# Performance work log

Hardware: AMD Instinct MI355X
Metric: run time of the kernel (lower is better)

Reference implementation:

```python
import jax, jax.numpy as jnp
import numpy as np

N_STATE, N_OBS, BATCH, T_LEN = 256, 128, 64, 1024
RICCATI_ITERS = 300


def _steady_state_gain(A, H, Q, R, iters=RICCATI_ITERS):
    """Riccati iteration for the steady-state Kalman gain (numpy, fp64)."""
    n = A.shape[0]
    I = np.eye(n)
    P = np.eye(n)
    for _ in range(iters):
        Pp = A @ P @ A.T + Q
        S = H @ Pp @ H.T + R
        K = np.linalg.solve(S, (Pp @ H.T).T).T
        P = (I - K @ H) @ Pp
    return K


def setup_inputs() -> dict:
    rng = np.random.default_rng(0)
    # Stable dynamics: scaled orthogonal matrix (spectral radius 0.95).
    M = rng.standard_normal((N_STATE, N_STATE))
    Qm, _ = np.linalg.qr(M)
    A = 0.95 * Qm
    H = rng.standard_normal((N_OBS, N_STATE)) / np.sqrt(N_STATE)
    Qc = 0.1 * np.eye(N_STATE)
    Rc = 0.1 * np.eye(N_OBS)
    K = _steady_state_gain(A, H, Qc, Rc)

    key = jax.random.key(0)
    y = jax.random.normal(key, (BATCH, T_LEN, N_OBS), dtype=jnp.float32)
    return {
        "y": y,
        "A": jnp.asarray(A, dtype=jnp.float32),
        "H": jnp.asarray(H, dtype=jnp.float32),
        "K": jnp.asarray(K, dtype=jnp.float32),
    }


def reference(y, A, H, K):
    """Steady-state Kalman filter: x_t = (I - K H) A x_{t-1} + K y_t.

    y: [B, T, n_obs] -> out: [B, T, n_state]
    """
    n = A.shape[0]
    I = jnp.eye(n, dtype=A.dtype)
    A_eff = (I - K @ H) @ A  # [n, n]

    x0 = y[:, 0] @ K.T  # [B, n]

    def step(x, yt):
        x = x @ A_eff.T + yt @ K.T  # [B, n]
        return x, x

    ys = jnp.swapaxes(y[:, 1:], 0, 1)  # [T-1, B, n_obs]
    _, xs = jax.lax.scan(step, x0, ys)  # xs: [T-1, B, n]
    out = jnp.concatenate([x0[:, None, :], jnp.swapaxes(xs, 0, 1)], axis=1)
    return out  # [B, T, n_state]
```

## Files before the change

### kernel.cpp

```cpp
#include <hip/hip_runtime.h>
#include <hip/hip_bf16.h>

#define NS 256
#define MO 128
#define BB 64
#define TT 1024
#define CCH 64
#define SS 16

typedef short s16x8 __attribute__((ext_vector_type(8)));
typedef float f32x4 __attribute__((ext_vector_type(4)));
typedef unsigned int uint;
typedef unsigned short ushort;

__device__ __forceinline__ ushort f2bf(float x) {
    uint u = __float_as_uint(x);
    uint r = (u + 0x7fffu + ((u >> 16) & 1u)) >> 16;
    return (ushort)r;
}
__device__ __forceinline__ float bf2f(ushort h) { return __uint_as_float(((uint)h) << 16); }

__device__ __forceinline__ uint pkbf2(float a, float b) {
    __hip_bfloat162 h = __float22bfloat162_rn(make_float2(a, b));
    union { __hip_bfloat162 b2; uint u; } cv;
    cv.b2 = h;
    return cv.u;
}

__device__ __forceinline__ void conv8(float4 f0, float4 f1, s16x8& vh, s16x8& vl) {
    uint h0 = pkbf2(f0.x, f0.y), h1 = pkbf2(f0.z, f0.w);
    uint h2 = pkbf2(f1.x, f1.y), h3 = pkbf2(f1.z, f1.w);
    float r0 = f0.x - __uint_as_float(h0 << 16);
    float r1 = f0.y - __uint_as_float(h0 & 0xffff0000u);
    float r2 = f0.z - __uint_as_float(h1 << 16);
    float r3 = f0.w - __uint_as_float(h1 & 0xffff0000u);
    float r4 = f1.x - __uint_as_float(h2 << 16);
    float r5 = f1.y - __uint_as_float(h2 & 0xffff0000u);
    float r6 = f1.z - __uint_as_float(h3 << 16);
    float r7 = f1.w - __uint_as_float(h3 & 0xffff0000u);
    uint l0 = pkbf2(r0, r1), l1 = pkbf2(r2, r3);
    uint l2 = pkbf2(r4, r5), l3 = pkbf2(r6, r7);
    union { uint u[4]; s16x8 v; } ch, cl;
    ch.u[0] = h0; ch.u[1] = h1; ch.u[2] = h2; ch.u[3] = h3;
    cl.u[0] = l0; cl.u[1] = l1; cl.u[2] = l2; cl.u[3] = l3;
    vh = ch.v; vl = cl.v;
}

__device__ __forceinline__ f32x4 mfma16(s16x8 a, s16x8 b, f32x4 c) {
    return __builtin_amdgcn_mfma_f32_16x16x32_bf16(a, b, c, 0, 0, 0);
}


__global__ void kh_kernel(const float* __restrict__ K, const float* __restrict__ H,
                          float* __restrict__ KH) {
    int i = blockIdx.x, j = threadIdx.x;
    __shared__ float kl[MO];
    if (j < MO) kl[j] = K[i * MO + j];
    __syncthreads();
    float acc = 0.f;
#pragma unroll 8
    for (int k = 0; k < MO; ++k) acc += kl[k] * H[k * NS + j];
    KH[i * NS + j] = acc;
}

__global__ void aeff_kernel(const float* __restrict__ A, const float* __restrict__ KH,
                            float* __restrict__ AE) {
    int i = blockIdx.x, j = threadIdx.x;
    __shared__ float khr[NS];
    khr[j] = KH[i * NS + j];
    __syncthreads();
    float acc = A[i * NS + j];
#pragma unroll 8
    for (int k = 0; k < NS; ++k) acc -= khr[k] * A[k * NS + j];
    AE[i * NS + j] = acc;
}

__global__ void matsq_kernel(const float* __restrict__ src, float* __restrict__ dst) {
    int i = blockIdx.x, j = threadIdx.x;
    __shared__ float row[NS];
    row[j] = src[i * NS + j];
    __syncthreads();
    float acc = 0.f;
#pragma unroll 8
    for (int k = 0; k < NS; ++k) acc += row[k] * src[k * NS + j];
    dst[i * NS + j] = acc;
}

__global__ void conv_kernel(const float* __restrict__ AE, const float* __restrict__ M,
                            const float* __restrict__ M2, const float* __restrict__ K,
                            ushort* __restrict__ aeh, ushort* __restrict__ ael,
                            ushort* __restrict__ mh, ushort* __restrict__ ml,
                            ushort* __restrict__ m2h, ushort* __restrict__ m2l,
                            ushort* __restrict__ kbh, ushort* __restrict__ kbl) {
    int blk = blockIdx.x;
    if (blk >= 768) {
        int i = (blk - 768) * 256 + threadIdx.x;
        float v = K[i];
        ushort hi = f2bf(v);
        kbh[i] = hi;
        kbl[i] = f2bf(v - bf2f(hi));
        return;
    }
    int i = (blk & 255) * 256 + threadIdx.x;
    int mat = blk >> 8;
    const float* src = (mat == 0) ? AE : ((mat == 1) ? M : M2);
    ushort* dh = (mat == 0) ? aeh : ((mat == 1) ? mh : m2h);
    ushort* dl = (mat == 0) ? ael : ((mat == 1) ? ml : m2l);
    float v = src[i];
    ushort hi = f2bf(v);
    dh[i] = hi;
    dl[i] = f2bf(v - bf2f(hi));
}


template <int MODE>
__launch_bounds__(512, 2)
__global__ void scan16_kernel(const ushort* __restrict__ mh, const ushort* __restrict__ ml,
                              const ushort* __restrict__ kbh, const ushort* __restrict__ kbl,
                              const float* __restrict__ y_g,
                              const float* u, const float* __restrict__ cin,
                              float* wout, float* __restrict__ eout) {
    constexpr bool YF = (MODE == 0 || MODE == 4);
    constexpr int S = YF ? SS : 8;
    const int tid = threadIdx.x;
    const int blk = blockIdx.x;
    const int w = tid >> 6;
    const int l = tid & 63;
    const int lr = l & 15;
    const int lg = l >> 4;

    __shared__ ushort xh_s[16 * NS];
    __shared__ ushort xl_s[16 * NS];
    __shared__ float ybuf[2][16 * MO];
    __shared__ float xe_s[16 * NS];

    const int b0 = (blk & 3) * 16;
    const int cc = blk >> 2;
    const int t0 = cc * SS;

    auto ubase = [&](int m) -> long {
        if constexpr (MODE == 1 || MODE == 3) {
            int rid = blk * 16 + m;
            int b = rid >> 3, g = rid & 7;
            return ((long)b * 64 + g * 8) * NS;
        } else {
            int b = blk * 16 + m;
            return (long)b * 8 * NS;
        }
    };

    s16x8 Bh[2][8], Bl[2][8];
#pragma unroll
    for (int t2 = 0; t2 < 2; ++t2) {
        int row = 16 * (2 * w + t2) + lr;
#pragma unroll
        for (int q = 0; q < 8; ++q) {
            int off = row * NS + 32 * q + 8 * lg;
            Bh[t2][q] = *(const s16x8*)(mh + off);
            Bl[t2][q] = *(const s16x8*)(ml + off);
        }
    }

    s16x8 KBh[2][4], KBl[2][4];
    if constexpr (YF) {
#pragma unroll
        for (int t2 = 0; t2 < 2; ++t2) {
            int row = 16 * (2 * w + t2) + lr;
#pragma unroll
            for (int q = 0; q < 4; ++q) {
                int off = row * MO + 32 * q + 8 * lg;
                KBh[t2][q] = *(const s16x8*)(kbh + off);
                KBl[t2][q] = *(const s16x8*)(kbl + off);
            }
        }
    }

#pragma unroll
    for (int jj = 0; jj < 8; ++jj) {
        int idx = jj * 512 + tid;
        int m = idx >> 8, col = idx & 255;
        float xv = 0.f;
        if constexpr (MODE == 3) {
            int rid = blk * 16 + m;
            int b = rid >> 3, g = rid & 7;
            xv = cin[(b * 8 + g) * NS + col];
            if (g == 0) wout[(long)b * 64 * NS + col] = 0.f;
        } else if constexpr (MODE == 4) {
            xv = cin[((long)(b0 + m) * 64 + cc) * NS + col];
        } else if constexpr (MODE == 2) {
            int b = blk * 16 + m;
            wout[(long)b * 8 * NS + col] = 0.f;
        }
        ushort hi = f2bf(xv);
        ushort lo = f2bf(xv - bf2f(hi));
        int sidx = (m * NS + col) ^ ((m & 7) << 3);
        xh_s[sidx] = hi;
        xl_s[sidx] = lo;
    }

    const int col0 = 32 * w + lr;
    const int col1 = col0 + 16;

    const int yr = tid >> 5;
    const int yc = (tid & 31) << 2;
    const float* ysrc = nullptr;
    int ywbyte = 0;
    float4 vnext = make_float4(0.f, 0.f, 0.f, 0.f);
    if constexpr (YF) {
        ysrc = y_g + ((size_t)(b0 + yr) * TT + t0) * MO + yc;
        ywbyte = (yr * 512 + yc * 4) ^ ((yr & 7) << 4);
        float4 v0 = *(const float4*)(ysrc);
        *(float4*)((char*)(&ybuf[0][0]) + ywbyte) = v0;
        vnext = *(const float4*)(ysrc + MO);
    }

    float up0[4], up1[4];
    if constexpr (!YF) {
#pragma unroll
        for (int i = 0; i < 4; ++i) {
            int m = 4 * lg + i;
            long ub = ubase(m);
            up0[i] = u[ub + col0];
            up1[i] = u[ub + col1];
        }
    }
    __syncthreads();

    for (int s = 0; s < S; ++s) {
        f32x4 acc0, acc1;
        if constexpr (YF) {
            acc0 = f32x4{0.f, 0.f, 0.f, 0.f};
            acc1 = f32x4{0.f, 0.f, 0.f, 0.f};
            const char* yb = (const char*)(&ybuf[s & 1][0]);
#pragma unroll
            for (int q = 0; q < 4; ++q) {
                int lb = lr * 512 + q * 128 + lg * 32;
                float4 f0 = *(const float4*)(yb + (lb ^ ((lr & 7) << 4)));
                float4 f1 = *(const float4*)(yb + ((lb + 16) ^ ((lr & 7) << 4)));
                s16x8 yh, yl;
                conv8(f0, f1, yh, yl);
                acc0 = mfma16(yh, KBh[0][q], acc0);
                acc0 = mfma16(yl, KBh[0][q], acc0);
                acc0 = mfma16(yh, KBl[0][q], acc0);
                acc1 = mfma16(yh, KBh[1][q], acc1);
                acc1 = mfma16(yl, KBh[1][q], acc1);
                acc1 = mfma16(yh, KBl[1][q], acc1);
            }
        } else {
            acc0[0] = up0[0]; acc0[1] = up0[1]; acc0[2] = up0[2]; acc0[3] = up0[3];
            acc1[0] = up1[0]; acc1[1] = up1[1]; acc1[2] = up1[2]; acc1[3] = up1[3];
        }

#pragma unroll
        for (int q = 0; q < 8; ++q) {
            int ridx = (lr * NS + 32 * q + 8 * lg) ^ ((lr & 7) << 3);
            s16x8 xh = *(const s16x8*)&xh_s[ridx];
            s16x8 xl = *(const s16x8*)&xl_s[ridx];
            acc0 = mfma16(xh, Bh[0][q], acc0);
            acc0 = mfma16(xl, Bh[0][q], acc0);
            acc0 = mfma16(xh, Bl[0][q], acc0);
            acc1 = mfma16(xh, Bh[1][q], acc1);
            acc1 = mfma16(xl, Bh[1][q], acc1);
            acc1 = mfma16(xh, Bl[1][q], acc1);
        }

        if constexpr (!YF) {
            if (s + 1 < S) {
#pragma unroll
                for (int i = 0; i < 4; ++i) {
                    int m = 4 * lg + i;
                    long ub = ubase(m) + (long)(s + 1) * NS;
                    up0[i] = u[ub + col0];
                    up1[i] = u[ub + col1];
                }
            }
        }

        if constexpr (MODE == 2) {
            if (s < 7) {
#pragma unroll
                for (int i = 0; i < 4; ++i) {
                    int m = 4 * lg + i;
                    int b = blk * 16 + m;
                    long wb = ((long)b * 8 + s + 1) * NS;
                    wout[wb + col0] = acc0[i];
                    wout[wb + col1] = acc1[i];
                }
            }
        } else if constexpr (MODE == 3) {
#pragma unroll
            for (int i = 0; i < 4; ++i) {
                int m = 4 * lg + i;
                int rid = blk * 16 + m;
                int b = rid >> 3, g = rid & 7;
                int kk = 8 * g + s + 1;
                if (kk < 64) {
                    long wb = ((long)b * 64 + kk) * NS;
                    wout[wb + col0] = acc0[i];
                    wout[wb + col1] = acc1[i];
                }
            }
        }
        if constexpr (MODE == 0 || MODE == 1) {
            if (s == S - 1) {
#pragma unroll
                for (int i = 0; i < 4; ++i) {
                    int m = 4 * lg + i;
                    long eb;
                    if constexpr (MODE == 0) {
                        eb = ((long)(b0 + m) * 64 + cc) * NS;
                    } else {
                        eb = (long)(blk * 16 + m) * NS;
                    }
                    eout[eb + col0] = acc0[i];
                    eout[eb + col1] = acc1[i];
                }
            }
        }

        __syncthreads();

#pragma unroll
        for (int i = 0; i < 4; ++i) {
            int m = 4 * lg + i;
            {
                ushort hi = f2bf(acc0[i]);
                ushort lo = f2bf(acc0[i] - bf2f(hi));
                int wi = (m * NS + col0) ^ ((m & 7) << 3);
                xh_s[wi] = hi;
                xl_s[wi] = lo;
            }
            {
                ushort hi = f2bf(acc1[i]);
                ushort lo = f2bf(acc1[i] - bf2f(hi));
                int wi = (m * NS + col1) ^ ((m & 7) << 3);
                xh_s[wi] = hi;
                xl_s[wi] = lo;
            }
            if constexpr (MODE == 4) {
                xe_s[(m * NS + col0) ^ ((m & 7) << 2)] = acc0[i];
                xe_s[(m * NS + col1) ^ ((m & 7) << 2)] = acc1[i];
            }
        }
        if constexpr (YF) {
            if (s + 1 < S) {
                *(float4*)((char*)(&ybuf[(s + 1) & 1][0]) + ywbyte) = vnext;
                if (s + 2 < S) vnext = *(const float4*)(ysrc + (size_t)(s + 2) * MO);
            }
        }
        __syncthreads();

        if constexpr (MODE == 4) {
#pragma unroll
            for (int j = 0; j < 2; ++j) {
                int idx = j * 512 + tid;
                int r = idx >> 6;
                int wb = idx << 2;
                float4 vv = *(const float4*)&xe_s[wb ^ ((r & 7) << 2)];
                long ob = ((long)(b0 + r) * TT + (t0 + s)) * NS + (wb & 255);
                *(float4*)(wout + ob) = vv;
            }
        }
    }
}


extern "C" void kernel_launch(void* const* d_in, const int* in_sizes, int n_in,
                              void* d_out, int out_size, void* d_ws, size_t ws_size,
                              hipStream_t stream) {
    const float* y = (const float*)d_in[0];
    const float* A = (const float*)d_in[1];
    const float* H = (const float*)d_in[2];
    const float* K = (const float*)d_in[3];
    float* out = (float*)d_out;

    float* ws = (float*)d_ws;
    const long MAT = (long)NS * NS;
    float* KH = ws + 0 * MAT;
    float* AE = ws + 1 * MAT;
    float* W0 = ws + 2 * MAT;
    float* W1 = ws + 3 * MAT;
    float* W2 = ws + 4 * MAT;
    float* W3 = ws + 5 * MAT;
    float* W4 = ws + 6 * MAT;
    float* W5 = ws + 7 * MAT;
    float* W6 = ws + 8 * MAT;
    ushort* aeh = (ushort*)(ws + 9 * MAT);
    ushort* ael = aeh + MAT;
    ushort* mh = ael + MAT;
    ushort* ml = mh + MAT;
    ushort* m2h = ml + MAT;
    ushort* m2l = m2h + MAT;
    ushort* kbh = (ushort*)(ws + 12 * MAT);
    ushort* kbl = kbh + (long)NS * MO;
    float* e_buf = ws + 13 * MAT;
    float* e2 = ws + 29 * MAT;
    float* c2 = ws + 31 * MAT;
    float* cbuf = ws + 33 * MAT;

    kh_kernel<<<NS, NS, 0, stream>>>(K, H, KH);
    aeff_kernel<<<NS, NS, 0, stream>>>(A, KH, AE);
    matsq_kernel<<<NS, NS, 0, stream>>>(AE, W0);
    matsq_kernel<<<NS, NS, 0, stream>>>(W0, W1);
    matsq_kernel<<<NS, NS, 0, stream>>>(W1, W2);
    matsq_kernel<<<NS, NS, 0, stream>>>(W2, W3);
    matsq_kernel<<<NS, NS, 0, stream>>>(W3, W4);
    matsq_kernel<<<NS, NS, 0, stream>>>(W4, W5);
    matsq_kernel<<<NS, NS, 0, stream>>>(W5, W6);
    conv_kernel<<<896, 256, 0, stream>>>(AE, W3, W6, K, aeh, ael, mh, ml, m2h, m2l, kbh, kbl);

    scan16_kernel<0><<<256, 512, 0, stream>>>(aeh, ael, kbh, kbl, y, nullptr, nullptr, nullptr, e_buf);
    scan16_kernel<1><<<32, 512, 0, stream>>>(mh, ml, nullptr, nullptr, nullptr, e_buf, nullptr, nullptr, e2);
    scan16_kernel<2><<<4, 512, 0, stream>>>(m2h, m2l, nullptr, nullptr, nullptr, e2, nullptr, c2, nullptr);
    scan16_kernel<3><<<32, 512, 0, stream>>>(mh, ml, nullptr, nullptr, nullptr, e_buf, c2, cbuf, nullptr);
    scan16_kernel<4><<<256, 512, 0, stream>>>(aeh, ael, kbh, kbl, y, nullptr, cbuf, out, nullptr);
}
```

Measured before the change: 272.4 us.

## Restructure hierarchical scan: precompute input GEMM, chunk of 8, bf16 carries, double-buffered LDS

```diff
diff --git a/kernel.cpp b/kernel.cpp
--- a/kernel.cpp
+++ b/kernel.cpp
@@ -5,8 +5,6 @@
 #define MO 128
 #define BB 64
 #define TT 1024
-#define CCH 64
-#define SS 16
 
 typedef short s16x8 __attribute__((ext_vector_type(8)));
 typedef float f32x4 __attribute__((ext_vector_type(4)));
@@ -52,10 +50,17 @@
 
 
 __global__ void kh_kernel(const float* __restrict__ K, const float* __restrict__ H,
-                          float* __restrict__ KH) {
+                          float* __restrict__ KH,
+                          ushort* __restrict__ kbh, ushort* __restrict__ kbl) {
     int i = blockIdx.x, j = threadIdx.x;
     __shared__ float kl[MO];
-    if (j < MO) kl[j] = K[i * MO + j];
+    if (j < MO) {
+        float v = K[i * MO + j];
+        kl[j] = v;
+        ushort hi = f2bf(v);
+        kbh[i * MO + j] = hi;
+        kbl[i * MO + j] = f2bf(v - bf2f(hi));
+    }
     __syncthreads();
     float acc = 0.f;
 #pragma unroll 8
@@ -64,7 +69,8 @@
 }
 
 __global__ void aeff_kernel(const float* __restrict__ A, const float* __restrict__ KH,
-                            float* __restrict__ AE) {
+                            float* __restrict__ AE,
+                            ushort* __restrict__ aeh, ushort* __restrict__ ael) {
     int i = blockIdx.x, j = threadIdx.x;
     __shared__ float khr[NS];
     khr[j] = KH[i * NS + j];
@@ -73,9 +79,13 @@
 #pragma unroll 8
     for (int k = 0; k < NS; ++k) acc -= khr[k] * A[k * NS + j];
     AE[i * NS + j] = acc;
-}
-
-__global__ void matsq_kernel(const float* __restrict__ src, float* __restrict__ dst) {
+    ushort hi = f2bf(acc);
+    aeh[i * NS + j] = hi;
+    ael[i * NS + j] = f2bf(acc - bf2f(hi));
+}
+
+__global__ void matsq_kernel(const float* __restrict__ src, float* __restrict__ dst,
+                             ushort* dh, ushort* dl) {
     int i = blockIdx.x, j = threadIdx.x;
     __shared__ float row[NS];
     row[j] = src[i * NS + j];
@@ -84,70 +94,91 @@
 #pragma unroll 8
     for (int k = 0; k < NS; ++k) acc += row[k] * src[k * NS + j];
     dst[i * NS + j] = acc;
-}
-
-__global__ void conv_kernel(const float* __restrict__ AE, const float* __restrict__ M,
-                            const float* __restrict__ M2, const float* __restrict__ K,
-                            ushort* __restrict__ aeh, ushort* __restrict__ ael,
-                            ushort* __restrict__ mh, ushort* __restrict__ ml,
-                            ushort* __restrict__ m2h, ushort* __restrict__ m2l,
-                            ushort* __restrict__ kbh, ushort* __restrict__ kbl) {
-    int blk = blockIdx.x;
-    if (blk >= 768) {
-        int i = (blk - 768) * 256 + threadIdx.x;
-        float v = K[i];
-        ushort hi = f2bf(v);
-        kbh[i] = hi;
-        kbl[i] = f2bf(v - bf2f(hi));
-        return;
-    }
-    int i = (blk & 255) * 256 + threadIdx.x;
-    int mat = blk >> 8;
-    const float* src = (mat == 0) ? AE : ((mat == 1) ? M : M2);
-    ushort* dh = (mat == 0) ? aeh : ((mat == 1) ? mh : m2h);
-    ushort* dl = (mat == 0) ? ael : ((mat == 1) ? ml : m2l);
-    float v = src[i];
-    ushort hi = f2bf(v);
-    dh[i] = hi;
-    dl[i] = f2bf(v - bf2f(hi));
+    if (dh) {
+        ushort hi = f2bf(acc);
+        dh[i * NS + j] = hi;
+        dl[i * NS + j] = f2bf(acc - bf2f(hi));
+    }
+}
+
+
+__launch_bounds__(512, 4)
+__global__ void ugemm_kernel(const float* __restrict__ y, const ushort* __restrict__ kbh,
+                             const ushort* __restrict__ kbl, float* __restrict__ U) {
+    const int tid = threadIdx.x, blk = blockIdx.x;
+    const int w = tid >> 6, l = tid & 63, lr = l & 15, lg = l >> 4;
+
+    __shared__ float xe[16 * NS];
+
+    s16x8 KBh[2][4], KBl[2][4];
+#pragma unroll
+    for (int t2 = 0; t2 < 2; ++t2) {
+        int row = 16 * (2 * w + t2) + lr;
+#pragma unroll
+        for (int q = 0; q < 4; ++q) {
+            int off = row * MO + 32 * q + 8 * lg;
+            KBh[t2][q] = *(const s16x8*)(kbh + off);
+            KBl[t2][q] = *(const s16x8*)(kbl + off);
+        }
+    }
+
+#pragma unroll 1
+    for (int it = 0; it < 8; ++it) {
+        long row0 = ((long)blk * 8 + it) * 16;
+        s16x8 Ah[4], Al[4];
+#pragma unroll
+        for (int q = 0; q < 4; ++q) {
+            long off = (row0 + lr) * MO + 32 * q + 8 * lg;
+            float4 f0 = *(const float4*)(y + off);
+            float4 f1 = *(const float4*)(y + off + 4);
+            conv8(f0, f1, Ah[q], Al[q]);
+        }
+        f32x4 acc0 = {0.f, 0.f, 0.f, 0.f};
+        f32x4 acc1 = {0.f, 0.f, 0.f, 0.f};
+#pragma unroll
+        for (int q = 0; q < 4; ++q) {
+            acc0 = mfma16(Ah[q], KBh[0][q], acc0);
+            acc0 = mfma16(Al[q], KBh[0][q], acc0);
+            acc0 = mfma16(Ah[q], KBl[0][q], acc0);
+            acc1 = mfma16(Ah[q], KBh[1][q], acc1);
+            acc1 = mfma16(Al[q], KBh[1][q], acc1);
+            acc1 = mfma16(Ah[q], KBl[1][q], acc1);
+        }
+        const int col0 = 32 * w + lr, col1 = col0 + 16;
+#pragma unroll
+        for (int i = 0; i < 4; ++i) {
+            int m = 4 * lg + i;
+            xe[(m * NS + col0) ^ ((m & 7) << 2)] = acc0[i];
+            xe[(m * NS + col1) ^ ((m & 7) << 2)] = acc1[i];
+        }
+        __syncthreads();
+#pragma unroll
+        for (int j = 0; j < 2; ++j) {
+            int idx = j * 512 + tid;
+            int r = idx >> 6;
+            int wb = idx << 2;
+            float4 v = *(const float4*)&xe[wb ^ ((r & 7) << 2)];
+            *(float4*)(U + (row0 + r) * NS + (wb & 255)) = v;
+        }
+        __syncthreads();
+    }
 }
 
 
 template <int MODE>
-__launch_bounds__(512, 2)
+__launch_bounds__(512, 4)
 __global__ void scan16_kernel(const ushort* __restrict__ mh, const ushort* __restrict__ ml,
-                              const ushort* __restrict__ kbh, const ushort* __restrict__ kbl,
-                              const float* __restrict__ y_g,
-                              const float* u, const float* __restrict__ cin,
-                              float* wout, float* __restrict__ eout) {
-    constexpr bool YF = (MODE == 0 || MODE == 4);
-    constexpr int S = YF ? SS : 8;
-    const int tid = threadIdx.x;
-    const int blk = blockIdx.x;
-    const int w = tid >> 6;
-    const int l = tid & 63;
-    const int lr = l & 15;
-    const int lg = l >> 4;
-
-    __shared__ ushort xh_s[16 * NS];
-    __shared__ ushort xl_s[16 * NS];
-    __shared__ float ybuf[2][16 * MO];
-    __shared__ float xe_s[16 * NS];
-
-    const int b0 = (blk & 3) * 16;
-    const int cc = blk >> 2;
-    const int t0 = cc * SS;
-
-    auto ubase = [&](int m) -> long {
-        if constexpr (MODE == 1 || MODE == 3) {
-            int rid = blk * 16 + m;
-            int b = rid >> 3, g = rid & 7;
-            return ((long)b * 64 + g * 8) * NS;
-        } else {
-            int b = blk * 16 + m;
-            return (long)b * 8 * NS;
-        }
-    };
+                              const float* __restrict__ uf, const ushort* __restrict__ ub,
+                              const ushort* __restrict__ cin, float* __restrict__ outf,
+                              ushort* __restrict__ wbf, ushort* __restrict__ ebf) {
+    constexpr int S = (MODE == 2) ? 15 : ((MODE == 3) ? 7 : 8);
+    constexpr bool UF32 = (MODE == 0 || MODE == 4);
+    const int tid = threadIdx.x, blk = blockIdx.x;
+    const int w = tid >> 6, l = tid & 63, lr = l & 15, lg = l >> 4;
+
+    __shared__ ushort xh_s[2][16 * NS];
+    __shared__ ushort xl_s[2][16 * NS];
+    __shared__ float xe_s[(MODE == 4) ? 2 * 16 * NS : 4];
 
     s16x8 Bh[2][8], Bl[2][8];
 #pragma unroll
@@ -161,101 +192,70 @@
         }
     }
 
-    s16x8 KBh[2][4], KBl[2][4];
-    if constexpr (YF) {
-#pragma unroll
-        for (int t2 = 0; t2 < 2; ++t2) {
-            int row = 16 * (2 * w + t2) + lr;
-#pragma unroll
-            for (int q = 0; q < 4; ++q) {
-                int off = row * MO + 32 * q + 8 * lg;
-                KBh[t2][q] = *(const s16x8*)(kbh + off);
-                KBl[t2][q] = *(const s16x8*)(kbl + off);
-            }
-        }
-    }
-
 #pragma unroll
     for (int jj = 0; jj < 8; ++jj) {
         int idx = jj * 512 + tid;
         int m = idx >> 8, col = idx & 255;
-        float xv = 0.f;
+        ushort hu = 0;
         if constexpr (MODE == 3) {
             int rid = blk * 16 + m;
-            int b = rid >> 3, g = rid & 7;
-            xv = cin[(b * 8 + g) * NS + col];
-            if (g == 0) wout[(long)b * 64 * NS + col] = 0.f;
+            int b = rid >> 4, g = rid & 15;
+            hu = cin[((long)b * 16 + g) * NS + col];
+            wbf[((long)b * 128 + g * 8) * NS + col] = hu;
         } else if constexpr (MODE == 4) {
-            xv = cin[((long)(b0 + m) * 64 + cc) * NS + col];
+            int b = (blk & 3) * 16 + m, cc = blk >> 2;
+            hu = cin[((long)b * 128 + cc) * NS + col];
         } else if constexpr (MODE == 2) {
             int b = blk * 16 + m;
-            wout[(long)b * 8 * NS + col] = 0.f;
-        }
-        ushort hi = f2bf(xv);
-        ushort lo = f2bf(xv - bf2f(hi));
-        int sidx = (m * NS + col) ^ ((m & 7) << 3);
-        xh_s[sidx] = hi;
-        xl_s[sidx] = lo;
-    }
-
-    const int col0 = 32 * w + lr;
-    const int col1 = col0 + 16;
-
-    const int yr = tid >> 5;
-    const int yc = (tid & 31) << 2;
-    const float* ysrc = nullptr;
-    int ywbyte = 0;
-    float4 vnext = make_float4(0.f, 0.f, 0.f, 0.f);
-    if constexpr (YF) {
-        ysrc = y_g + ((size_t)(b0 + yr) * TT + t0) * MO + yc;
-        ywbyte = (yr * 512 + yc * 4) ^ ((yr & 7) << 4);
-        float4 v0 = *(const float4*)(ysrc);
-        *(float4*)((char*)(&ybuf[0][0]) + ywbyte) = v0;
-        vnext = *(const float4*)(ysrc + MO);
+            wbf[(long)b * 16 * NS + col] = 0;
+        }
+        int si = (m * NS + col) ^ ((m & 7) << 3);
+        xh_s[0][si] = hu;
+        xl_s[0][si] = 0;
+    }
+
+    const int col0 = 32 * w + lr, col1 = col0 + 16;
+    const int m0 = 4 * lg;
+
+    long ubo[4];
+#pragma unroll
+    for (int i = 0; i < 4; ++i) {
+        int m = m0 + i;
+        if constexpr (UF32) {
+            int b = (blk & 3) * 16 + m, cc = blk >> 2;
+            ubo[i] = ((long)b * TT + cc * 8) * NS;
+        } else if constexpr (MODE == 1 || MODE == 3) {
+            int rid = blk * 16 + m;
+            ubo[i] = ((long)(rid >> 4) * 128 + (rid & 15) * 8) * NS;
+        } else {
+            ubo[i] = (long)(blk * 16 + m) * 16 * NS;
+        }
     }
 
     float up0[4], up1[4];
-    if constexpr (!YF) {
-#pragma unroll
-        for (int i = 0; i < 4; ++i) {
-            int m = 4 * lg + i;
-            long ub = ubase(m);
-            up0[i] = u[ub + col0];
-            up1[i] = u[ub + col1];
+#pragma unroll
+    for (int i = 0; i < 4; ++i) {
+        if constexpr (UF32) {
+            up0[i] = uf[ubo[i] + col0];
+            up1[i] = uf[ubo[i] + col1];
+        } else {
+            up0[i] = bf2f(ub[ubo[i] + col0]);
+            up1[i] = bf2f(ub[ubo[i] + col1]);
         }
     }
     __syncthreads();
 
     for (int s = 0; s < S; ++s) {
+        const int cur = s & 1, nxt = cur ^ 1;
         f32x4 acc0, acc1;
-        if constexpr (YF) {
-            acc0 = f32x4{0.f, 0.f, 0.f, 0.f};
-            acc1 = f32x4{0.f, 0.f, 0.f, 0.f};
-            const char* yb = (const char*)(&ybuf[s & 1][0]);
-#pragma unroll
-            for (int q = 0; q < 4; ++q) {
-                int lb = lr * 512 + q * 128 + lg * 32;
-                float4 f0 = *(const float4*)(yb + (lb ^ ((lr & 7) << 4)));
-                float4 f1 = *(const float4*)(yb + ((lb + 16) ^ ((lr & 7) << 4)));
-                s16x8 yh, yl;
-                conv8(f0, f1, yh, yl);
-                acc0 = mfma16(yh, KBh[0][q], acc0);
-                acc0 = mfma16(yl, KBh[0][q], acc0);
-                acc0 = mfma16(yh, KBl[0][q], acc0);
-                acc1 = mfma16(yh, KBh[1][q], acc1);
-                acc1 = mfma16(yl, KBh[1][q], acc1);
-                acc1 = mfma16(yh, KBl[1][q], acc1);
-            }
-        } else {
-            acc0[0] = up0[0]; acc0[1] = up0[1]; acc0[2] = up0[2]; acc0[3] = up0[3];
-            acc1[0] = up1[0]; acc1[1] = up1[1]; acc1[2] = up1[2]; acc1[3] = up1[3];
-        }
+        acc0[0] = up0[0]; acc0[1] = up0[1]; acc0[2] = up0[2]; acc0[3] = up0[3];
+        acc1[0] = up1[0]; acc1[1] = up1[1]; acc1[2] = up1[2]; acc1[3] = up1[3];
 
 #pragma unroll
         for (int q = 0; q < 8; ++q) {
             int ridx = (lr * NS + 32 * q + 8 * lg) ^ ((lr & 7) << 3);
-            s16x8 xh = *(const s16x8*)&xh_s[ridx];
-            s16x8 xl = *(const s16x8*)&xl_s[ridx];
+            s16x8 xh = *(const s16x8*)&xh_s[cur][ridx];
+            s16x8 xl = *(const s16x8*)&xl_s[cur][ridx];
             acc0 = mfma16(xh, Bh[0][q], acc0);
             acc0 = mfma16(xl, Bh[0][q], acc0);
             acc0 = mfma16(xh, Bl[0][q], acc0);
@@ -264,101 +264,93 @@
             acc1 = mfma16(xh, Bl[1][q], acc1);
         }
 
-        if constexpr (!YF) {
-            if (s + 1 < S) {
+        if (s + 1 < S) {
+#pragma unroll
+            for (int i = 0; i < 4; ++i) {
+                long ue = ubo[i] + (long)(s + 1) * NS;
+                if constexpr (UF32) {
+                    up0[i] = uf[ue + col0];
+                    up1[i] = uf[ue + col1];
+                } else {
+                    up0[i] = bf2f(ub[ue + col0]);
+                    up1[i] = bf2f(ub[ue + col1]);
+                }
+            }
+        }
+
+        if constexpr (MODE == 2) {
+#pragma unroll
+            for (int i = 0; i < 4; ++i) {
+                int b = blk * 16 + m0 + i;
+                long wb = ((long)b * 16 + s + 1) * NS;
+                wbf[wb + col0] = f2bf(acc0[i]);
+                wbf[wb + col1] = f2bf(acc1[i]);
+            }
+        } else if constexpr (MODE == 3) {
+#pragma unroll
+            for (int i = 0; i < 4; ++i) {
+                int rid = blk * 16 + m0 + i;
+                int b = rid >> 4, g = rid & 15;
+                long wb = ((long)b * 128 + g * 8 + s + 1) * NS;
+                wbf[wb + col0] = f2bf(acc0[i]);
+                wbf[wb + col1] = f2bf(acc1[i]);
+            }
+        } else if constexpr (MODE == 0) {
+            if (s == S - 1) {
 #pragma unroll
                 for (int i = 0; i < 4; ++i) {
-                    int m = 4 * lg + i;
-                    long ub = ubase(m) + (long)(s + 1) * NS;
-                    up0[i] = u[ub + col0];
-                    up1[i] = u[ub + col1];
+                    int b = (blk & 3) * 16 + m0 + i, cc = blk >> 2;
+                    long eb = ((long)b * 128 + cc) * NS;
+                    ebf[eb + col0] = f2bf(acc0[i]);
+                    ebf[eb + col1] = f2bf(acc1[i]);
                 }
             }
-        }
-
-        if constexpr (MODE == 2) {
-            if (s < 7) {
+        } else if constexpr (MODE == 1) {
+            if (s == S - 1) {
 #pragma unroll
                 for (int i = 0; i < 4; ++i) {
-                    int m = 4 * lg + i;
-                    int b = blk * 16 + m;
-                    long wb = ((long)b * 8 + s + 1) * NS;
-                    wout[wb + col0] = acc0[i];
-                    wout[wb + col1] = acc1[i];
+                    int rid = blk * 16 + m0 + i;
+                    long eb = ((long)(rid >> 4) * 16 + (rid & 15)) * NS;
+                    ebf[eb + col0] = f2bf(acc0[i]);
+                    ebf[eb + col1] = f2bf(acc1[i]);
                 }
             }
-        } else if constexpr (MODE == 3) {
-#pragma unroll
-            for (int i = 0; i < 4; ++i) {
-                int m = 4 * lg + i;
-                int rid = blk * 16 + m;
-                int b = rid >> 3, g = rid & 7;
-                int kk = 8 * g + s + 1;
-                if (kk < 64) {
-                    long wb = ((long)b * 64 + kk) * NS;
-                    wout[wb + col0] = acc0[i];
-                    wout[wb + col1] = acc1[i];
-                }
-            }
-        }
-        if constexpr (MODE == 0 || MODE == 1) {
-            if (s == S - 1) {
-#pragma unroll
-                for (int i = 0; i < 4; ++i) {
-                    int m = 4 * lg + i;
-                    long eb;
-                    if constexpr (MODE == 0) {
-                        eb = ((long)(b0 + m) * 64 + cc) * NS;
-                    } else {
-                        eb = (long)(blk * 16 + m) * NS;
-                    }
-                    eout[eb + col0] = acc0[i];
-                    eout[eb + col1] = acc1[i];
-                }
-            }
-        }
-
-        __syncthreads();
+        }
 
 #pragma unroll
         for (int i = 0; i < 4; ++i) {
-            int m = 4 * lg + i;
+            int m = m0 + i;
             {
                 ushort hi = f2bf(acc0[i]);
                 ushort lo = f2bf(acc0[i] - bf2f(hi));
                 int wi = (m * NS + col0) ^ ((m & 7) << 3);
-                xh_s[wi] = hi;
-                xl_s[wi] = lo;
+                xh_s[nxt][wi] = hi;
+                xl_s[nxt][wi] = lo;
             }
             {
                 ushort hi = f2bf(acc1[i]);
                 ushort lo = f2bf(acc1[i] - bf2f(hi));
                 int wi = (m * NS + col1) ^ ((m & 7) << 3);
-                xh_s[wi] = hi;
-                xl_s[wi] = lo;
+                xh_s[nxt][wi] = hi;
+                xl_s[nxt][wi] = lo;
             }
             if constexpr (MODE == 4) {
-                xe_s[(m * NS + col0) ^ ((m & 7) << 2)] = acc0[i];
-                xe_s[(m * NS + col1) ^ ((m & 7) << 2)] = acc1[i];
-            }
-        }
-        if constexpr (YF) {
-            if (s + 1 < S) {
-                *(float4*)((char*)(&ybuf[(s + 1) & 1][0]) + ywbyte) = vnext;
-                if (s + 2 < S) vnext = *(const float4*)(ysrc + (size_t)(s + 2) * MO);
+                xe_s[cur * 4096 + ((m * NS + col0) ^ ((m & 7) << 2))] = acc0[i];
+                xe_s[cur * 4096 + ((m * NS + col1) ^ ((m & 7) << 2))] = acc1[i];
             }
         }
         __syncthreads();
 
         if constexpr (MODE == 4) {
+            const int t = (blk >> 2) * 8 + s;
 #pragma unroll
             for (int j = 0; j < 2; ++j) {
                 int idx = j * 512 + tid;
                 int r = idx >> 6;
                 int wb = idx << 2;
-                float4 vv = *(const float4*)&xe_s[wb ^ ((r & 7) << 2)];
-                long ob = ((long)(b0 + r) * TT + (t0 + s)) * NS + (wb & 255);
-                *(float4*)(wout + ob) = vv;
+                float4 v = *(const float4*)&xe_s[cur * 4096 + (wb ^ ((r & 7) << 2))];
+                long ob = ((long)((blk & 3) * 16 + r) * TT + t) * NS + (wb & 255);
+                *(float4*)(outf + ob) = v;
             }
         }
     }
@@ -378,40 +370,39 @@
     const long MAT = (long)NS * NS;
     float* KH = ws + 0 * MAT;
     float* AE = ws + 1 * MAT;
-    float* W0 = ws + 2 * MAT;
-    float* W1 = ws + 3 * MAT;
-    float* W2 = ws + 4 * MAT;
-    float* W3 = ws + 5 * MAT;
-    float* W4 = ws + 6 * MAT;
-    float* W5 = ws + 7 * MAT;
-    float* W6 = ws + 8 * MAT;
-    ushort* aeh = (ushort*)(ws + 9 * MAT);
+    float* Ta = ws + 2 * MAT;
+    float* Tb = ws + 3 * MAT;
+    float* M8 = ws + 4 * MAT;
+    float* M64 = ws + 5 * MAT;
+    ushort* aeh = (ushort*)(ws + 6 * MAT);
     ushort* ael = aeh + MAT;
-    ushort* mh = ael + MAT;
+    ushort* mh = (ushort*)(ws + 7 * MAT);
     ushort* ml = mh + MAT;
-    ushort* m2h = ml + MAT;
+    ushort* m2h = (ushort*)(ws + 8 * MAT);
     ushort* m2l = m2h + MAT;
-    ushort* kbh = (ushort*)(ws + 12 * MAT);
+    ushort* kbh = (ushort*)(ws + 9 * MAT);
     ushort* kbl = kbh + (long)NS * MO;
-    float* e_buf = ws + 13 * MAT;
-    float* e2 = ws + 29 * MAT;
-    float* c2 = ws + 31 * MAT;
-    float* cbuf = ws + 33 * MAT;
-
-    kh_kernel<<<NS, NS, 0, stream>>>(K, H, KH);
-    aeff_kernel<<<NS, NS, 0, stream>>>(A, KH, AE);
-    matsq_kernel<<<NS, NS, 0, stream>>>(AE, W0);
-    matsq_kernel<<<NS, NS, 0, stream>>>(W0, W1);
-    matsq_kernel<<<NS, NS, 0, stream>>>(W1, W2);
-    matsq_kernel<<<NS, NS, 0, stream>>>(W2, W3);
-    matsq_kernel<<<NS, NS, 0, stream>>>(W3, W4);
-    matsq_kernel<<<NS, NS, 0, stream>>>(W4, W5);
-    matsq_kernel<<<NS, NS, 0, stream>>>(W5, W6);
-    conv_kernel<<<896, 256, 0, stream>>>(AE, W3, W6, K, aeh, ael, mh, ml, m2h, m2l, kbh, kbl);
-
-    scan16_kernel<0><<<256, 512, 0, stream>>>(aeh, ael, kbh, kbl, y, nullptr, nullptr, nullptr, e_buf);
-    scan16_kernel<1><<<32, 512, 0, stream>>>(mh, ml, nullptr, nullptr, nullptr, e_buf, nullptr, nullptr, e2);
-    scan16_kernel<2><<<4, 512, 0, stream>>>(m2h, m2l, nullptr, nullptr, nullptr, e2, nullptr, c2, nullptr);
-    scan16_kernel<3><<<32, 512, 0, stream>>>(mh, ml, nullptr, nullptr, nullptr, e_buf, c2, cbuf, nullptr);
-    scan16_kernel<4><<<256, 512, 0, stream>>>(aeh, ael, kbh, kbl, y, nullptr, cbuf, out, nullptr);
-}
+    ushort* e_buf = (ushort*)(ws + 10 * MAT);
+    ushort* cbuf = (ushort*)(ws + 26 * MAT);
+    ushort* e2 = (ushort*)(ws + 42 * MAT);
+    ushort* c2 = (ushort*)(ws + 44 * MAT);
+
+    float* U = out;
+
+    kh_kernel<<<NS, NS, 0, stream>>>(K, H, KH, kbh, kbl);
+    aeff_kernel<<<NS, NS, 0, stream>>>(A, KH, AE, aeh, ael);
+    matsq_kernel<<<NS, NS, 0, stream>>>(AE, Ta, nullptr, nullptr);
+    matsq_kernel<<<NS, NS, 0, stream>>>(Ta, Tb, nullptr, nullptr);
+    matsq_kernel<<<NS, NS, 0, stream>>>(Tb, M8, mh, ml);
+    matsq_kernel<<<NS, NS, 0, stream>>>(M8, Ta, nullptr, nullptr);
+    matsq_kernel<<<NS, NS, 0, stream>>>(Ta, Tb, nullptr, nullptr);
+    matsq_kernel<<<NS, NS, 0, stream>>>(Tb, M64, m2h, m2l);
+
+    ugemm_kernel<<<512, 512, 0, stream>>>(y, kbh, kbl, U);
+
+    scan16_kernel<0><<<512, 512, 0, stream>>>(aeh, ael, U, nullptr, nullptr, nullptr, nullptr, e_buf);
+    scan16_kernel<1><<<64, 512, 0, stream>>>(mh, ml, nullptr, e_buf, nullptr, nullptr, nullptr, e2);
+    scan16_kernel<2><<<4, 512, 0, stream>>>(m2h, m2l, nullptr, e2, nullptr, nullptr, c2, nullptr);
+    scan16_kernel<3><<<64, 512, 0, stream>>>(mh, ml, nullptr, e_buf, c2, nullptr, cbuf, nullptr);
+    scan16_kernel<4><<<512, 512, 0, stream>>>(aeh, ael, U, nullptr, cbuf, out, nullptr, nullptr);
+}
```

Result: slower. 471.0 us (+72.9%).
